# Kernel tuning notes

Hardware: AMD Instinct MI355X
Metric: run time of the kernel (lower is better)

Reference implementation:

```python
import jax, jax.numpy as jnp
import numpy as np

N, D, C = 8192, 512, 16
HM, HG = 256, 64  # mlp hidden, gcn hidden
ENHANCE = 6.0
LW0, LW1 = 1.0, 1.0  # loss_weight
NEG = jnp.float32(-9e15)


def setup_inputs() -> dict:
    key = jax.random.key(0)
    ks = jax.random.split(key, 12)
    feature = jax.random.normal(ks[0], (N, D), dtype=jnp.float32)
    # sparse symmetric binary adjacency with self loops (avg degree ~ 65)
    A = (jax.random.uniform(ks[1], (N, N)) < 0.004).astype(jnp.float32)
    adj = jnp.maximum(jnp.maximum(A, A.T), jnp.eye(N, dtype=jnp.float32))
    node_labels = jax.random.randint(ks[2], (N,), 0, C)
    labels_oneHot = jax.nn.one_hot(node_labels, C, dtype=jnp.float32)
    bias = jnp.ones((C, C), jnp.float32) + (ENHANCE - 1.0) * jnp.eye(C, dtype=jnp.float32)
    s = 0.05
    Wm1 = s * jax.random.normal(ks[3], (D, HM), dtype=jnp.float32)
    bm1 = jnp.zeros((HM,), jnp.float32)
    Wm2 = s * jax.random.normal(ks[4], (HM, C), dtype=jnp.float32)
    bm2 = jnp.zeros((C,), jnp.float32)
    W1 = s * jax.random.normal(ks[5], (D, HG), dtype=jnp.float32)
    b1 = jnp.zeros((HG,), jnp.float32)
    W2 = s * jax.random.normal(ks[6], (HG, C), dtype=jnp.float32)
    b2 = jnp.zeros((C,), jnp.float32)
    idx = jax.random.randint(ks[7], (1024,), 0, N)
    label = node_labels[idx]
    mask = jax.random.randint(ks[8], (N,), 0, 2).astype(bool)  # train mask
    return {"feature": feature, "adj": adj, "labels_oneHot": labels_oneHot,
            "bias": bias, "Wm1": Wm1, "bm1": bm1, "Wm2": Wm2, "bm2": bm2,
            "W1": W1, "b1": b1, "W2": W2, "b2": b2,
            "idx": idx, "label": label, "mask": mask}


def reference(feature, adj, labels_oneHot, bias, Wm1, bm1, Wm2, bm2,
              W1, b1, W2, b2, idx, label, mask):
    # MLP soft labels B: [N, C]
    B = jax.nn.softmax(jnp.maximum(feature @ Wm1 + bm1, 0.0) @ Wm2 + bm2, axis=1)
    # block matrix H: ground truth labels on train nodes, soft labels elsewhere
    soft_y = jnp.where(mask[:, None], labels_oneHot, B)          # [N, C]
    Hm = soft_y.T @ adj                                          # [C, N]
    H = (Hm @ soft_y) / jnp.sum(Hm, axis=1, keepdims=True)       # [C, C]
    Q = (H @ H.T) * bias
    Q = Q / jnp.sum(Q, axis=1, keepdims=True)                    # [C, C]
    # edge score B Q B^T, adjacency-masked softmax
    score = (B @ Q @ B.T) * adj                                  # [N, N]
    g = jax.nn.softmax(jnp.where(adj > 0, score, NEG), axis=1)   # [N, N]
    # 2-layer GCN with g as propagation matrix
    h = jnp.maximum(g @ (feature @ W1) + b1, 0.0)                # [N, HG]
    output = g @ (h @ W2) + b2                                   # [N, C]
    logits = jax.nn.softmax(output, axis=1)
    gcn_loss = -jnp.mean(jnp.log(logits[idx, label]))
    mlp_loss = -jnp.mean(jnp.log(B[idx, label]))
    final_loss = LW0 * gcn_loss + LW1 * mlp_loss
    return logits, final_loss, jax.lax.stop_gradient(H), jax.lax.stop_gradient(Q), jax.lax.stop_gradient(output)
```

## Files before the change

kernel.cpp:

```cpp
#include <hip/hip_runtime.h>
#include <math.h>

#define N   8192
#define D   512
#define C   16
#define HM  256
#define HG  64
#define KMAX 128

typedef __attribute__((ext_vector_type(8))) short bf16x8;
typedef __attribute__((ext_vector_type(4))) float f32x4;
typedef unsigned long long ull;

__device__ __forceinline__ unsigned short f2b(float x) {
  union { float f; unsigned int u; } v; v.f = x;
  unsigned int r = v.u + 0x7FFFu + ((v.u >> 16) & 1u);
  return (unsigned short)(r >> 16);
}
__device__ __forceinline__ float b2f(unsigned short b) {
  union { unsigned int u; float f; } v; v.u = ((unsigned int)b) << 16;
  return v.f;
}

__global__ __launch_bounds__(256) void prep_kernel(const float* __restrict__ feat,
    const float* __restrict__ Wm1, const float* __restrict__ W1,
    const float* __restrict__ Wm2, unsigned short* __restrict__ Abf,
    unsigned short* __restrict__ Wt, unsigned short* __restrict__ Wm2tb) {
  const int tid = blockIdx.x * 256 + threadIdx.x;
  const float4 a = *(const float4*)&feat[(size_t)tid * 8];
  const float4 b = *(const float4*)&feat[(size_t)tid * 8 + 4];
  ushort4 lo, hi;
  lo.x = f2b(a.x); lo.y = f2b(a.y); lo.z = f2b(a.z); lo.w = f2b(a.w);
  hi.x = f2b(b.x); hi.y = f2b(b.y); hi.z = f2b(b.z); hi.w = f2b(b.w);
  *(ushort4*)&Abf[(size_t)tid * 8] = lo;
  *(ushort4*)&Abf[(size_t)tid * 8 + 4] = hi;
  if (tid < 320 * 512) {
    const int n = tid >> 9, k = tid & 511;
    const float v = (n < 256) ? Wm1[k * 256 + n] : W1[k * 64 + (n - 256)];
    Wt[tid] = f2b(v);
  }
  if (tid < 16 * 256) {
    const int cc = tid >> 8, k = tid & 255;
    Wm2tb[tid] = f2b(Wm2[k * 16 + cc]);
  }
}

__global__ __launch_bounds__(256) void tile_ballot(const float* __restrict__ adj,
    ull* __restrict__ bm) {
  const int I = blockIdx.y, J = blockIdx.x;
  if (J < I) return;
  __shared__ unsigned char tb[64][68];
  const int t = threadIdx.x;
  #pragma unroll
  for (int rr = 0; rr < 4; ++rr) {
    const int r = rr * 16 + (t >> 4);
    const int c = (t & 15) * 4;
    const float4 v = *(const float4*)&adj[(size_t)(I * 64 + r) * N + J * 64 + c];
    tb[r][c + 0] = v.x > 0.f;
    tb[r][c + 1] = v.y > 0.f;
    tb[r][c + 2] = v.z > 0.f;
    tb[r][c + 3] = v.w > 0.f;
  }
  __syncthreads();
  const int lane = t & 63, w = t >> 6;
  #pragma unroll
  for (int i = 0; i < 16; ++i) {
    const int r = w * 16 + i;
    const ull rw = __ballot(tb[r][lane] != 0);
    if (lane == 0) bm[(size_t)(I * 64 + r) * 128 + J] = rw;
    const ull cw = __ballot(tb[lane][r] != 0);
    if (lane == 0) bm[(size_t)(J * 64 + r) * 128 + I] = cw;
  }
}

__global__ __launch_bounds__(256) void gemm_mlp(
    const bf16x8* __restrict__ Abf, const bf16x8* __restrict__ Wt,
    const float* __restrict__ bm1, const bf16x8* __restrict__ Wm2tb,
    const float* __restrict__ bm2, const float* __restrict__ labels1h,
    const int* __restrict__ mask, float* __restrict__ Bmat,
    float* __restrict__ softy, unsigned short* __restrict__ X1b) {
  __shared__ unsigned short c1[32][264];
  const int l = threadIdx.x & 63, w = threadIdx.x >> 6;
  const int m0 = blockIdx.x * 32;
  const int kb = l >> 4, cl = l & 15;
  const int rw = (w >> 1) * 16;
  const int nt0 = (w & 1) * 10;
  const int row = m0 + rw + cl;
  const bf16x8* arow = Abf + (size_t)row * 64 + kb;
  f32x4 acc[10] = {};
  for (int kk = 0; kk < 16; ++kk) {
    const bf16x8 af = arow[kk * 4];
    #pragma unroll
    for (int i = 0; i < 10; ++i) {
      const bf16x8 bfr = Wt[(size_t)((nt0 + i) * 16 + cl) * 64 + kk * 4 + kb];
      acc[i] = __builtin_amdgcn_mfma_f32_16x16x32_bf16(af, bfr, acc[i], 0, 0, 0);
    }
  }
  const int rl0 = rw + kb * 4;
  #pragma unroll
  for (int i = 0; i < 10; ++i) {
    const int nt = nt0 + i;
    const int col = nt * 16 + cl;
    if (nt < 16) {
      const float bv = bm1[col];
      #pragma unroll
      for (int r = 0; r < 4; ++r)
        c1[rl0 + r][col] = f2b(fmaxf(acc[i][r] + bv, 0.f));
    } else {
      const int xc = col - 256;
      #pragma unroll
      for (int r = 0; r < 4; ++r)
        X1b[(size_t)(m0 + rl0 + r) * HG + xc] = f2b(acc[i][r]);
    }
  }
  __syncthreads();
  if ((w & 1) == 0) {
    f32x4 acc2 = {0.f, 0.f, 0.f, 0.f};
    #pragma unroll
    for (int kk = 0; kk < 8; ++kk) {
      const bf16x8 a2 = *(const bf16x8*)&c1[rw + cl][kk * 32 + kb * 8];
      const bf16x8 b2v = Wm2tb[(size_t)cl * 32 + kk * 4 + kb];
      acc2 = __builtin_amdgcn_mfma_f32_16x16x32_bf16(a2, b2v, acc2, 0, 0, 0);
    }
    const float bm2v = bm2[cl];
    #pragma unroll
    for (int r = 0; r < 4; ++r) {
      float v = acc2[r] + bm2v;
      float m = v;
      #pragma unroll
      for (int s = 1; s < 16; s <<= 1) m = fmaxf(m, __shfl_xor(m, s));
      const float e = __expf(v - m);
      float ssum = e;
      #pragma unroll
      for (int s = 1; s < 16; s <<= 1) ssum += __shfl_xor(ssum, s);
      const float bb = e / ssum;
      const int grow = m0 + rw + kb * 4 + r;
      Bmat[grow * C + cl] = bb;
      softy[grow * C + cl] = mask[grow] ? labels1h[grow * C + cl] : bb;
    }
  }
}

__global__ __launch_bounds__(256) void extract_nbr(const ull* __restrict__ bm,
    int* __restrict__ rowcnt, int* __restrict__ colidx,
    const float* __restrict__ softy, float* __restrict__ nbrsum) {
  __shared__ int cs[4][128];
  const int t = threadIdx.x, lane = t & 63, w = t >> 6;
  const int row = blockIdx.x * 4 + w;
  const ull w0 = bm[(size_t)row * 128 + lane];
  const ull w1 = bm[(size_t)row * 128 + 64 + lane];
  const int c0 = __builtin_popcountll(w0);
  const int c1 = __builtin_popcountll(w1);
  int s0 = c0, s1 = c1;
  #pragma unroll
  for (int s = 1; s < 64; s <<= 1) {
    const int y0 = __shfl_up(s0, s);
    const int y1 = __shfl_up(s1, s);
    if (lane >= s) { s0 += y0; s1 += y1; }
  }
  const int total0 = __shfl(s0, 63);
  const int total = total0 + __shfl(s1, 63);
  int off = s0 - c0;
  ull x = w0;
  while (x) {
    const int b = __builtin_ctzll(x);
    if (off < KMAX) {
      const int col = lane * 64 + b;
      colidx[(size_t)row * KMAX + off] = col;
      cs[w][off] = col;
    }
    ++off;
    x &= x - 1;
  }
  off = total0 + s1 - c1;
  x = w1;
  while (x) {
    const int b = __builtin_ctzll(x);
    if (off < KMAX) {
      const int col = (64 + lane) * 64 + b;
      colidx[(size_t)row * KMAX + off] = col;
      cs[w][off] = col;
    }
    ++off;
    x &= x - 1;
  }
  const int cnt = min(total, KMAX);
  if (lane == 0) rowcnt[row] = cnt;
  __syncthreads();
  const int cc = lane & 15, grp = lane >> 4;
  float acc = 0.f;
  for (int e = grp; e < cnt; e += 4)
    acc += softy[cs[w][e] * C + cc];
  acc += __shfl_xor(acc, 16);
  acc += __shfl_xor(acc, 32);
  if (lane < 16) nbrsum[row * C + cc] = acc;
}

__global__ __launch_bounds__(256) void h_partial(const float* __restrict__ nbrsum,
    const float* __restrict__ softy, float* __restrict__ Hpart) {
  const int t = threadIdx.x;
  const int c = t >> 4, cp = t & 15;
  float acc = 0.f, dacc = 0.f;
  const int j0 = blockIdx.x * (N / 64);
  for (int j = j0; j < j0 + N / 64; ++j) {
    const float nv = nbrsum[j * C + c];
    acc = fmaf(nv, softy[j * C + cp], acc);
    if (cp == 0) dacc += nv;
  }
  Hpart[blockIdx.x * 272 + t] = acc;
  if (cp == 0) Hpart[blockIdx.x * 272 + 256 + c] = dacc;
}

__global__ __launch_bounds__(256) void hq_final(const float* __restrict__ Hpart,
    const float* __restrict__ bias, float* __restrict__ H_out,
    float* __restrict__ Q_out, float* __restrict__ Qws) {
  __shared__ float Hs[256], Qs[256], rs[16], dd[16];
  const int t = threadIdx.x;
  const int c = t >> 4, cp = t & 15;
  float acc = 0.f;
  for (int b = 0; b < 64; ++b) acc += Hpart[b * 272 + t];
  if (t < 16) {
    float s = 0.f;
    for (int b = 0; b < 64; ++b) s += Hpart[b * 272 + 256 + t];
    dd[t] = s;
  }
  __syncthreads();
  const float Hv = acc / dd[c];
  Hs[t] = Hv;
  H_out[t] = Hv;
  __syncthreads();
  float q = 0.f;
  for (int k = 0; k < 16; ++k) q = fmaf(Hs[c * 16 + k], Hs[cp * 16 + k], q);
  q *= bias[t];
  Qs[t] = q;
  __syncthreads();
  if (t < 16) {
    float s = 0.f;
    for (int k = 0; k < 16; ++k) s += Qs[t * 16 + k];
    rs[t] = s;
  }
  __syncthreads();
  const float Qv = q / rs[c];
  Q_out[t] = Qv;
  Qws[t] = Qv;
}

__global__ __launch_bounds__(256) void edge_gcn1(const float* __restrict__ Bmat,
    const float* __restrict__ Q, const int* __restrict__ rowcnt,
    const int* __restrict__ colidx, const unsigned short* __restrict__ X1b,
    const float* __restrict__ b1, const float* __restrict__ W2,
    float* __restrict__ gval, float* __restrict__ X2) {
  __shared__ float Prow[4][16];
  __shared__ float gv[4][128];
  __shared__ int cs[4][128];
  const int lane = threadIdx.x & 63, w = threadIdx.x >> 6;
  const int row = blockIdx.x * 4 + w;
  const int c = lane & 15, grp = lane >> 4;
  float acc = 0.f;
  for (int k = grp * 4; k < grp * 4 + 4; ++k)
    acc = fmaf(Bmat[row * C + k], Q[k * C + c], acc);
  acc += __shfl_xor(acc, 16);
  acc += __shfl_xor(acc, 32);
  if (lane < 16) Prow[w][c] = acc;
  __syncthreads();
  const int cnt = rowcnt[row];
  const int col0 = (lane < cnt) ? colidx[row * KMAX + lane] : 0;
  const int col1 = (lane + 64 < cnt) ? colidx[row * KMAX + lane + 64] : 0;
  float s0 = -1e30f, s1 = -1e30f;
  if (lane < cnt) {
    float s = 0.f;
    for (int k = 0; k < 16; ++k) s = fmaf(Prow[w][k], Bmat[col0 * C + k], s);
    s0 = s;
  }
  if (lane + 64 < cnt) {
    float s = 0.f;
    for (int k = 0; k < 16; ++k) s = fmaf(Prow[w][k], Bmat[col1 * C + k], s);
    s1 = s;
  }
  float m = fmaxf(s0, s1);
  for (int s = 1; s < 64; s <<= 1) m = fmaxf(m, __shfl_xor(m, s));
  const float e0 = __expf(s0 - m), e1 = __expf(s1 - m);
  float ssum = e0 + e1;
  for (int s = 1; s < 64; s <<= 1) ssum += __shfl_xor(ssum, s);
  const float inv = 1.f / ssum;
  const float g0 = e0 * inv, g1 = e1 * inv;
  if (lane < cnt) gval[row * KMAX + lane] = g0;
  if (lane + 64 < cnt) gval[row * KMAX + lane + 64] = g1;
  gv[w][lane] = g0; gv[w][lane + 64] = g1;
  cs[w][lane] = col0; cs[w][lane + 64] = col1;
  __syncthreads();
  float hacc = 0.f;
  for (int e = 0; e < cnt; ++e)
    hacc = fmaf(gv[w][e], b2f(X1b[(size_t)cs[w][e] * HG + lane]), hacc);
  const float h = fmaxf(hacc + b1[lane], 0.f);
  float x[16];
  #pragma unroll
  for (int cc = 0; cc < 16; ++cc) x[cc] = h * W2[lane * C + cc];
  #pragma unroll
  for (int s = 1; s < 64; s <<= 1)
    #pragma unroll
    for (int cc = 0; cc < 16; ++cc) x[cc] += __shfl_xor(x[cc], s);
  float v = x[0];
  #pragma unroll
  for (int cc = 1; cc < 16; ++cc) v = (lane == cc) ? x[cc] : v;
  if (lane < 16) X2[row * C + lane] = v;
}

__global__ __launch_bounds__(256) void gcn2(const float* __restrict__ X2,
    const float* __restrict__ b2, const int* __restrict__ rowcnt,
    const int* __restrict__ colidx, const float* __restrict__ gval,
    float* __restrict__ out_logits, float* __restrict__ out_output) {
  const int lane = threadIdx.x & 63;
  const int row = blockIdx.x * 4 + (threadIdx.x >> 6);
  const int c = lane & 15, grp = lane >> 4;
  const int cnt = rowcnt[row];
  float acc = 0.f;
  for (int e = grp; e < cnt; e += 4)
    acc = fmaf(gval[row * KMAX + e], X2[colidx[row * KMAX + e] * C + c], acc);
  acc += __shfl_xor(acc, 16);
  acc += __shfl_xor(acc, 32);
  acc += b2[c];
  float m = acc;
  for (int s = 1; s < 16; s <<= 1) m = fmaxf(m, __shfl_xor(m, s));
  const float e = __expf(acc - m);
  float ssum = e;
  for (int s = 1; s < 16; s <<= 1) ssum += __shfl_xor(ssum, s);
  if (lane < 16) {
    out_output[row * C + c] = acc;
    out_logits[row * C + c] = e / ssum;
  }
}

__global__ __launch_bounds__(256) void loss_kernel(const float* __restrict__ logits,
    const float* __restrict__ Bmat, const int* __restrict__ idx,
    const int* __restrict__ label, float* __restrict__ out_loss) {
  __shared__ float sg[256], sm[256];
  const int t = threadIdx.x;
  float g = 0.f, m = 0.f;
  for (int i = t; i < 1024; i += 256) {
    const int ii = idx[i], ll = label[i];
    g -= logf(logits[ii * C + ll]);
    m -= logf(Bmat[ii * C + ll]);
  }
  sg[t] = g; sm[t] = m;
  __syncthreads();
  for (int s = 128; s > 0; s >>= 1) {
    if (t < s) { sg[t] += sg[t + s]; sm[t] += sm[t + s]; }
    __syncthreads();
  }
  if (t == 0) out_loss[0] = 1.0f * (sg[0] / 1024.f) + 1.0f * (sm[0] / 1024.f);
}

extern "C" void kernel_launch(void* const* d_in, const int* in_sizes, int n_in,
                              void* d_out, int out_size, void* d_ws, size_t ws_size,
                              hipStream_t stream) {
  const float* feature  = (const float*)d_in[0];
  const float* adj      = (const float*)d_in[1];
  const float* labels1h = (const float*)d_in[2];
  const float* bias     = (const float*)d_in[3];
  const float* Wm1 = (const float*)d_in[4];
  const float* bm1 = (const float*)d_in[5];
  const float* Wm2 = (const float*)d_in[6];
  const float* bm2 = (const float*)d_in[7];
  const float* W1  = (const float*)d_in[8];
  const float* b1  = (const float*)d_in[9];
  const float* W2  = (const float*)d_in[10];
  const float* b2  = (const float*)d_in[11];
  const int* idx   = (const int*)d_in[12];
  const int* label = (const int*)d_in[13];
  const int* mask  = (const int*)d_in[14];

  float* out = (float*)d_out;
  float* logits_o = out;
  float* loss_o   = out + (size_t)N * C;
  float* H_o      = loss_o + 1;
  float* Q_o      = H_o + 256;
  float* outp_o   = Q_o + 256;

  float* p = (float*)d_ws;
  float* Bmat   = p; p += (size_t)N * C;
  float* softy  = p; p += (size_t)N * C;
  float* nbrsum = p; p += (size_t)N * C;
  float* X2     = p; p += (size_t)N * C;
  float* Hpart  = p; p += 64 * 272;
  float* Qws    = p; p += 256;
  int* rowcnt = (int*)p; p += N;
  int* colidx = (int*)p; p += (size_t)N * KMAX;
  float* gval = p; p += (size_t)N * KMAX;
  unsigned short* X1b   = (unsigned short*)p; p += (size_t)N * HG / 2;
  unsigned short* Abf   = (unsigned short*)p; p += (size_t)N * D / 2;
  unsigned short* Wt    = (unsigned short*)p; p += 320 * 512 / 2;
  unsigned short* Wm2tb = (unsigned short*)p; p += 16 * 256 / 2;
  ull* bm = (ull*)p;

  prep_kernel<<<(N * D / 8) / 256, 256, 0, stream>>>(feature, Wm1, W1, Wm2, Abf, Wt, Wm2tb);
  tile_ballot<<<dim3(128, 128), 256, 0, stream>>>(adj, bm);
  gemm_mlp<<<N / 32, 256, 0, stream>>>((const bf16x8*)Abf, (const bf16x8*)Wt, bm1,
      (const bf16x8*)Wm2tb, bm2, labels1h, mask, Bmat, softy, X1b);
  extract_nbr<<<N / 4, 256, 0, stream>>>(bm, rowcnt, colidx, softy, nbrsum);
  h_partial<<<64, 256, 0, stream>>>(nbrsum, softy, Hpart);
  hq_final<<<1, 256, 0, stream>>>(Hpart, bias, H_o, Q_o, Qws);
  edge_gcn1<<<N / 4, 256, 0, stream>>>(Bmat, Qws, rowcnt, colidx, X1b, b1, W2, gval, X2);
  gcn2<<<N / 4, 256, 0, stream>>>(X2, b2, rowcnt, colidx, gval, logits_o, outp_o);
  loss_kernel<<<1, 256, 0, stream>>>(logits_o, Bmat, idx, label, loss_o);
}
```

Measured before the change: 142.4 us.

## Fold weight prep into tile_ballot, convert features in GEMM, compact triangular grid

Removes the separate prep kernel. Weight transposition and bf16 conversion move into an extra row of blocks in the adjacency ballot kernel, and the fp32 feature matrix is now read and converted to bf16 inside the MLP GEMM loop. The ballot grid is reshaped from a 128x128 launch with half the blocks exiting early into a 129x65 launch that maps each block to an upper-triangular tile pair. This saves one launch plus a full write and re-read of the bf16 feature copy, but the GEMM now loads twice the bytes per feature element and does the conversion in its inner loop.

```diff
diff --git a/kernel.cpp b/kernel.cpp
--- a/kernel.cpp
+++ b/kernel.cpp
@@ -22,35 +22,28 @@
   return v.f;
 }
 
-__global__ __launch_bounds__(256) void prep_kernel(const float* __restrict__ feat,
-    const float* __restrict__ Wm1, const float* __restrict__ W1,
-    const float* __restrict__ Wm2, unsigned short* __restrict__ Abf,
-    unsigned short* __restrict__ Wt, unsigned short* __restrict__ Wm2tb) {
-  const int tid = blockIdx.x * 256 + threadIdx.x;
-  const float4 a = *(const float4*)&feat[(size_t)tid * 8];
-  const float4 b = *(const float4*)&feat[(size_t)tid * 8 + 4];
-  ushort4 lo, hi;
-  lo.x = f2b(a.x); lo.y = f2b(a.y); lo.z = f2b(a.z); lo.w = f2b(a.w);
-  hi.x = f2b(b.x); hi.y = f2b(b.y); hi.z = f2b(b.z); hi.w = f2b(b.w);
-  *(ushort4*)&Abf[(size_t)tid * 8] = lo;
-  *(ushort4*)&Abf[(size_t)tid * 8 + 4] = hi;
-  if (tid < 320 * 512) {
-    const int n = tid >> 9, k = tid & 511;
-    const float v = (n < 256) ? Wm1[k * 256 + n] : W1[k * 64 + (n - 256)];
-    Wt[tid] = f2b(v);
-  }
-  if (tid < 16 * 256) {
-    const int cc = tid >> 8, k = tid & 255;
-    Wm2tb[tid] = f2b(Wm2[k * 16 + cc]);
-  }
-}
-
 __global__ __launch_bounds__(256) void tile_ballot(const float* __restrict__ adj,
-    ull* __restrict__ bm) {
-  const int I = blockIdx.y, J = blockIdx.x;
-  if (J < I) return;
+    ull* __restrict__ bm, const float* __restrict__ Wm1, const float* __restrict__ W1,
+    const float* __restrict__ Wm2, unsigned short* __restrict__ Wt,
+    unsigned short* __restrict__ Wm2tb) {
+  const int t = threadIdx.x;
+  if (blockIdx.y == 64) {
+    const int start = blockIdx.x * 256 + t;
+    for (int i = start; i < 320 * 512; i += 129 * 256) {
+      const int n = i >> 9, k = i & 511;
+      Wt[i] = f2b((n < 256) ? Wm1[k * 256 + n] : W1[k * 64 + (n - 256)]);
+    }
+    for (int i = start; i < 16 * 256; i += 129 * 256) {
+      const int cc = i >> 8, k = i & 255;
+      Wm2tb[i] = f2b(Wm2[k * 16 + cc]);
+    }
+    return;
+  }
+  const int p = blockIdx.y;
+  int I, J;
+  if ((int)blockIdx.x < 128 - p) { I = p; J = p + blockIdx.x; }
+  else                           { I = 127 - p; J = blockIdx.x - 1; }
   __shared__ unsigned char tb[64][68];
-  const int t = threadIdx.x;
   #pragma unroll
   for (int rr = 0; rr < 4; ++rr) {
     const int r = rr * 16 + (t >> 4);
@@ -74,7 +67,7 @@
 }
 
 __global__ __launch_bounds__(256) void gemm_mlp(
-    const bf16x8* __restrict__ Abf, const bf16x8* __restrict__ Wt,
+    const float* __restrict__ feature, const bf16x8* __restrict__ Wt,
     const float* __restrict__ bm1, const bf16x8* __restrict__ Wm2tb,
     const float* __restrict__ bm2, const float* __restrict__ labels1h,
     const int* __restrict__ mask, float* __restrict__ Bmat,
@@ -86,10 +79,14 @@
   const int rw = (w >> 1) * 16;
   const int nt0 = (w & 1) * 10;
   const int row = m0 + rw + cl;
-  const bf16x8* arow = Abf + (size_t)row * 64 + kb;
+  const float* arow = feature + (size_t)row * D + kb * 8;
   f32x4 acc[10] = {};
   for (int kk = 0; kk < 16; ++kk) {
-    const bf16x8 af = arow[kk * 4];
+    const float4 a0 = *(const float4*)&arow[kk * 32];
+    const float4 a1 = *(const float4*)&arow[kk * 32 + 4];
+    bf16x8 af;
+    af[0] = f2b(a0.x); af[1] = f2b(a0.y); af[2] = f2b(a0.z); af[3] = f2b(a0.w);
+    af[4] = f2b(a1.x); af[5] = f2b(a1.y); af[6] = f2b(a1.z); af[7] = f2b(a1.w);
     #pragma unroll
     for (int i = 0; i < 10; ++i) {
       const bf16x8 bfr = Wt[(size_t)((nt0 + i) * 16 + cl) * 64 + kk * 4 + kb];
@@ -388,14 +385,12 @@
   int* colidx = (int*)p; p += (size_t)N * KMAX;
   float* gval = p; p += (size_t)N * KMAX;
   unsigned short* X1b   = (unsigned short*)p; p += (size_t)N * HG / 2;
-  unsigned short* Abf   = (unsigned short*)p; p += (size_t)N * D / 2;
   unsigned short* Wt    = (unsigned short*)p; p += 320 * 512 / 2;
   unsigned short* Wm2tb = (unsigned short*)p; p += 16 * 256 / 2;
   ull* bm = (ull*)p;
 
-  prep_kernel<<<(N * D / 8) / 256, 256, 0, stream>>>(feature, Wm1, W1, Wm2, Abf, Wt, Wm2tb);
-  tile_ballot<<<dim3(128, 128), 256, 0, stream>>>(adj, bm);
-  gemm_mlp<<<N / 32, 256, 0, stream>>>((const bf16x8*)Abf, (const bf16x8*)Wt, bm1,
+  tile_ballot<<<dim3(129, 65), 256, 0, stream>>>(adj, bm, Wm1, W1, Wm2, Wt, Wm2tb);
+  gemm_mlp<<<N / 32, 256, 0, stream>>>(feature, (const bf16x8*)Wt, bm1,
       (const bf16x8*)Wm2tb, bm2, labels1h, mask, Bmat, softy, X1b);
   extract_nbr<<<N / 4, 256, 0, stream>>>(bm, rowcnt, colidx, softy, nbrsum);
   h_partial<<<64, 256, 0, stream>>>(nbrsum, softy, Hpart);
```

Measured after the change: 126.9 us. 1.12x faster.
